# Kernel optimization log

Hardware: AMD Instinct MI355X
Metric: run time of the kernel (lower is better)

The kernel has to match this reference:

```python
import jax, jax.numpy as jnp
import numpy as np

V = 100000   # nodes
E = 3200000  # edges (avg degree 32)
K = 16       # radial filters
T = 4        # atom types


def setup_inputs() -> dict:
    key = jax.random.key(0)
    k1, k2, k3, k4 = jax.random.split(key, 4)
    feat = jax.random.randint(k1, (V, 1), 0, T).astype(jnp.float32)  # atomic-type ids as floats
    distances = jax.random.uniform(k2, (E, 1), jnp.float32) * 12.0   # pairwise distances in [0, 12)
    src = jax.random.randint(k3, (E,), 0, V, dtype=jnp.int32)
    dst = jax.random.randint(k4, (E,), 0, V, dtype=jnp.int32)
    interaction_cutoffs = jnp.full((K,), 12.0, dtype=jnp.float32)
    rbf_kernel_means = jnp.linspace(0.0, 12.0, K).astype(jnp.float32)
    rbf_kernel_scaling = jnp.ones((K,), dtype=jnp.float32)
    features_to_use = jnp.arange(T, dtype=jnp.float32)
    return {
        'feat': feat, 'distances': distances, 'src': src, 'dst': dst,
        'interaction_cutoffs': interaction_cutoffs,
        'rbf_kernel_means': rbf_kernel_means,
        'rbf_kernel_scaling': rbf_kernel_scaling,
        'features_to_use': features_to_use,
    }


def reference(feat, distances, src, dst, interaction_cutoffs,
              rbf_kernel_means, rbf_kernel_scaling, features_to_use):
    d = distances                                    # (E, 1)
    # RadialPooling: rbf * cosine cutoff, broadcast (E,1) vs (K,) -> (E,K)
    rbf = jnp.exp(-rbf_kernel_scaling * (d - rbf_kernel_means) ** 2)
    cos_v = 0.5 * (jnp.cos(jnp.pi * d / interaction_cutoffs) + 1.0)
    he = rbf * jnp.where(d <= interaction_cutoffs, cos_v, jnp.zeros_like(cos_v))  # (E, K)
    # one-hot atom-type features (V, T)
    hv = (feat == features_to_use[None, :]).astype(distances.dtype)
    # gather src features, outer product with radial features -> (E, T, K)
    msg = hv[src][:, :, None] * he[:, None, :]
    # scatter-sum to destination nodes -> (V, T*K)
    out = jax.ops.segment_sum(msg.reshape(msg.shape[0], -1), dst, num_segments=V)
    return out
```

## Files before the change

### kernel.cpp

```cpp
#include <hip/hip_runtime.h>
#include <math.h>

#define NV 100000
#define NE 3200000
#define NK 16
#define NT 4
#define NB 1563
#define NBP 1564
#define NKEY 256
#define SCH 4096
#define NCH ((NE + SCH - 1) / SCH)
#define RCAP 2432
#define CPT 4
#define NBIN 16384
#define BINSCALE (NBIN / 12.0f)
#define NVW ((NV + 15) / 16)
#define PI_F 3.14159265358979323846f

typedef float vfloat4 __attribute__((ext_vector_type(4)));
typedef int   vint4   __attribute__((ext_vector_type(4)));


__global__ __launch_bounds__(256) void zero_out_kernel(float4* __restrict__ out, int n4) {
    int i = blockIdx.x * blockDim.x + threadIdx.x;
    if (i < n4) out[i] = make_float4(0.f, 0.f, 0.f, 0.f);
}

__global__ __launch_bounds__(256) void atomic_conv_edge_kernel(
    const float* __restrict__ feat, const float* __restrict__ dist,
    const int* __restrict__ src, const int* __restrict__ dst,
    const float* __restrict__ cutoffs, const float* __restrict__ means,
    const float* __restrict__ scaling, const float* __restrict__ feats_use,
    float* __restrict__ out)
{
    int e = blockIdx.x * blockDim.x + threadIdx.x;
    if (e >= NE) return;
    float d = dist[e];
    int s = src[e];
    int v = dst[e];
    float fv = feat[s];
    int ty = 0;
#pragma unroll
    for (int t = 1; t < NT; ++t) if (fv == feats_use[t]) ty = t;
    float* o = out + (size_t)v * (NT * NK) + (size_t)ty * NK;
#pragma unroll
    for (int k = 0; k < NK; ++k) {
        float c = cutoffs[k], m = means[k], sc = scaling[k];
        float dm = d - m;
        float rbf = __expf(-sc * dm * dm);
        float cosv = 0.5f * (__cosf(PI_F * d / c) + 1.0f);
        float he = (d <= c) ? rbf * cosv : 0.0f;
        __hip_atomic_fetch_add(o + k, he, __ATOMIC_RELAXED, __HIP_MEMORY_SCOPE_AGENT);
    }
}


__global__ __launch_bounds__(256) void prep_kernel(
    const float* __restrict__ feat, const float* __restrict__ feats_use,
    const float* __restrict__ cutoffs, const float* __restrict__ means,
    const float* __restrict__ scaling,
    unsigned* __restrict__ fpk, float* __restrict__ tab)
{
    int tid = blockIdx.x * 256 + threadIdx.x;
    if (tid < NBIN * NK) {
        int bin = tid >> 4, k = tid & 15;
        float dc = ((float)bin + 0.5f) * (12.0f / NBIN);
        float c = cutoffs[k], m = means[k], sc = scaling[k];
        float dm = dc - m;
        float rbf = expf(-sc * dm * dm);
        float cosv = 0.5f * (cosf(PI_F * dc / c) + 1.0f);
        tab[tid] = (dc <= c) ? rbf * cosv : 0.0f;
    }
    if (tid < NVW) {
        float f1 = feats_use[1], f2 = feats_use[2], f3 = feats_use[3];
        unsigned w = 0;
        int base = tid * 16;
#pragma unroll
        for (int j = 0; j < 16; ++j) {
            int idx = base + j;
            float fv = (idx < NV) ? feat[idx] : -1.0f;
            unsigned ty = (fv == f1) ? 1u : (fv == f2) ? 2u : (fv == f3) ? 3u : 0u;
            w |= ty << (2 * j);
        }
        fpk[tid] = w;
    }
}


__global__ __launch_bounds__(512, 4) void scatter_kernel(
    const unsigned* __restrict__ fpk, const float* __restrict__ dist,
    const int* __restrict__ src, const int* __restrict__ dst,
    unsigned short* __restrict__ offs, unsigned* __restrict__ payload)
{
    __shared__ unsigned pld[SCH];
    __shared__ unsigned short bkt[SCH];
    __shared__ int hist[NB];
    __shared__ int wsum[8];

    int t = threadIdx.x;
    int c = blockIdx.x;
    int chunkBase = c * SCH;
    int n = NE - chunkBase;
    if (n > SCH) n = SCH;

    for (int i = t; i < NB; i += 512) hist[i] = 0;
    __syncthreads();

    int nq = n >> 2;
    const vfloat4* d4 = (const vfloat4*)(dist + chunkBase);
    const vint4*   s4 = (const vint4*)(src + chunkBase);
    const vint4*   v4 = (const vint4*)(dst + chunkBase);
    for (int i = t; i < nq; i += 512) {
        vfloat4 dd = __builtin_nontemporal_load(&d4[i]);
        vint4   ss = __builtin_nontemporal_load(&s4[i]);
        vint4   vv = __builtin_nontemporal_load(&v4[i]);
#pragma unroll
        for (int j = 0; j < 4; ++j) {
            int s = ss[j];
            unsigned w = fpk[s >> 4];
            unsigned ty = (w >> ((s & 15) << 1)) & 3u;
            int bin = (int)(dd[j] * BINSCALE);
            bin = (bin > NBIN - 1) ? NBIN - 1 : bin;
            int v = vv[j];
            pld[4 * i + j] = ((unsigned)bin << 8) | ((unsigned)(v & 63) << 2) | ty;
            bkt[4 * i + j] = (unsigned short)(v >> 6);
            atomicAdd(&hist[v >> 6], 1);
        }
    }
    for (int i = (nq << 2) + t; i < n; i += 512) {
        int e = chunkBase + i;
        int s = src[e];
        unsigned w = fpk[s >> 4];
        unsigned ty = (w >> ((s & 15) << 1)) & 3u;
        int bin = (int)(dist[e] * BINSCALE);
        bin = (bin > NBIN - 1) ? NBIN - 1 : bin;
        int v = dst[e];
        pld[i] = ((unsigned)bin << 8) | ((unsigned)(v & 63) << 2) | ty;
        bkt[i] = (unsigned short)(v >> 6);
        atomicAdd(&hist[v >> 6], 1);
    }
    __syncthreads();

    int base_i = t * CPT;
    int loc[CPT];
    int sum = 0;
#pragma unroll
    for (int i = 0; i < CPT; ++i) {
        int idx = base_i + i;
        int v = (idx < NB) ? hist[idx] : 0;
        loc[i] = sum;
        sum += v;
    }
    int lane = t & 63, wv = t >> 6;
    int inc = sum;
#pragma unroll
    for (int o = 1; o < 64; o <<= 1) {
        int u = __shfl_up(inc, o, 64);
        if (lane >= o) inc += u;
    }
    if (lane == 63) wsum[wv] = inc;
    __syncthreads();
    int add = 0;
#pragma unroll
    for (int w = 0; w < 8; ++w) add += (w < wv) ? wsum[w] : 0;
    int excl = add + inc - sum;

    unsigned short* __restrict__ oc = offs + (size_t)c * NBP;
#pragma unroll
    for (int i = 0; i < CPT; ++i) {
        int idx = base_i + i;
        int pref = excl + loc[i];
        if (idx < NB) {
            oc[idx] = (unsigned short)pref;
            hist[idx] = pref;
        } else if (idx == NB) {
            oc[NB] = (unsigned short)n;
        }
    }
    __syncthreads();

    unsigned* __restrict__ pout = payload + (size_t)chunkBase;
    for (int i = t; i < n; i += 512) {
        int b = bkt[i];
        int pos = atomicAdd(&hist[b], 1);
        pout[pos] = pld[i];
    }
}

__global__ __launch_bounds__(512, 8) void reduce_kernel(
    const unsigned* __restrict__ payload, const unsigned short* __restrict__ offs,
    const float* __restrict__ tab, float* __restrict__ out)
{
    __shared__ unsigned lds_buf[2 * RCAP];
    __shared__ int scn[NKEY];
    __shared__ int cur[NKEY];
    __shared__ int coff[NKEY + 1];
    __shared__ int wsum[4];
    __shared__ int tot;

    unsigned* raw = lds_buf;
    unsigned* srt = lds_buf + RCAP;
    float* stage = (float*)lds_buf;

    int jj = blockIdx.x;
    int xg = jj & 7, ji = jj >> 3;
    int b = ((xg < 3) ? xg * 196 : 588 + (xg - 3) * 195) + ji;
    int t = threadIdx.x;

    if (t < NKEY) scn[t] = 0;
    if (t == 0) tot = 0;
    __syncthreads();

    for (int c = t; c < NCH; c += 512) {
        const unsigned short* oc = offs + (size_t)c * NBP + b;
        int s = oc[0];
        int e = oc[1];
        int cnt = e - s;
        if (cnt > 0) {
            int pos = atomicAdd(&tot, cnt);
            if (pos + cnt > RCAP) cnt = (pos < RCAP) ? (RCAP - pos) : 0;
            const unsigned* __restrict__ pp = payload + (size_t)c * SCH + s;
            for (int q = 0; q < cnt; ++q) {
                unsigned p = pp[q];
                raw[pos + q] = p;
                atomicAdd(&scn[p & 255u], 1);
            }
        }
    }
    __syncthreads();
    int n = tot;
    if (n > RCAP) n = RCAP;

    int x = (t < NKEY) ? scn[t] : 0;
    int lane = t & 63, wv = t >> 6;
    int inc = x;
#pragma unroll
    for (int o = 1; o < 64; o <<= 1) {
        int u = __shfl_up(inc, o, 64);
        if (lane >= o) inc += u;
    }
    if (lane == 63 && t < NKEY) wsum[wv] = inc;
    __syncthreads();
    if (t < NKEY) {
        int add = 0;
#pragma unroll
        for (int w = 0; w < 4; ++w) add += (w < wv) ? wsum[w] : 0;
        int excl = add + inc - x;
        coff[t] = excl;
        cur[t] = excl;
        if (t == 255) coff[NKEY] = n;
    }
    __syncthreads();

    for (int i = t; i < n; i += 512) {
        unsigned p = raw[i];
        int pos = atomicAdd(&cur[p & 255u], 1);
        srt[pos] = p;
    }
    __syncthreads();

    float acc[NK];
#pragma unroll
    for (int k = 0; k < NK; ++k) acc[k] = 0.f;

    int key = t & 255;
    int s0 = coff[key];
    int s1 = coff[key + 1];
    int h = (s1 - s0) >> 1;
    int i0 = (t < NKEY) ? s0 : (s1 - h);
    int i1 = (t < NKEY) ? (s1 - h) : s1;

#pragma unroll 2
    for (int i = i0; i < i1; ++i) {
        unsigned p = srt[i];
        const vfloat4* row = (const vfloat4*)(tab + (size_t)((p >> 8) & 0x3FFFu) * 16);
        vfloat4 r0 = row[0], r1 = row[1], r2 = row[2], r3 = row[3];
        acc[0]  += r0.x; acc[1]  += r0.y; acc[2]  += r0.z; acc[3]  += r0.w;
        acc[4]  += r1.x; acc[5]  += r1.y; acc[6]  += r1.z; acc[7]  += r1.w;
        acc[8]  += r2.x; acc[9]  += r2.y; acc[10] += r2.z; acc[11] += r2.w;
        acc[12] += r3.x; acc[13] += r3.y; acc[14] += r3.z; acc[15] += r3.w;
    }
    __syncthreads();

    if (t >= NKEY) {
#pragma unroll
        for (int k = 0; k < NK; ++k) stage[(t - NKEY) * 17 + k] = acc[k];
    }
    __syncthreads();

    if (t < NKEY) {
#pragma unroll
        for (int k = 0; k < NK; ++k) acc[k] += stage[t * 17 + k];
        int node = b * 64 + (t >> 2);
        if (node < NV) {
            vfloat4* o = (vfloat4*)(out + (size_t)node * 64 + (size_t)(t & 3) * 16);
#pragma unroll
            for (int q = 0; q < 4; ++q) {
                vfloat4 v = {acc[4 * q], acc[4 * q + 1], acc[4 * q + 2], acc[4 * q + 3]};
                __builtin_nontemporal_store(v, &o[q]);
            }
        }
    }
}

extern "C" void kernel_launch(void* const* d_in, const int* in_sizes, int n_in,
                              void* d_out, int out_size, void* d_ws, size_t ws_size,
                              hipStream_t stream) {
    const float* feat      = (const float*)d_in[0];
    const float* dist      = (const float*)d_in[1];
    const int*   src       = (const int*)d_in[2];
    const int*   dst       = (const int*)d_in[3];
    const float* cutoffs   = (const float*)d_in[4];
    const float* means     = (const float*)d_in[5];
    const float* scaling   = (const float*)d_in[6];
    const float* feats_use = (const float*)d_in[7];
    float* out = (float*)d_out;

    size_t off = 0;
    auto alloc = [&](size_t bytes) {
        size_t cur = off;
        off = (off + bytes + 255) & ~(size_t)255;
        return cur;
    };
    size_t o_offs    = alloc((size_t)NCH * NBP * 2);
    size_t o_payload = alloc((size_t)NE * 4);
    size_t o_fpk     = alloc((size_t)NVW * 4);
    size_t o_tab     = alloc((size_t)NBIN * NK * 4);
    size_t needed = off;

    if (ws_size < needed) {
        int n4 = out_size / 4;
        zero_out_kernel<<<(n4 + 255) / 256, 256, 0, stream>>>((float4*)out, n4);
        atomic_conv_edge_kernel<<<(NE + 255) / 256, 256, 0, stream>>>(
            feat, dist, src, dst, cutoffs, means, scaling, feats_use, out);
        return;
    }

    char* ws = (char*)d_ws;
    unsigned short* offs = (unsigned short*)(ws + o_offs);
    unsigned* payload    = (unsigned*)(ws + o_payload);
    unsigned* fpk        = (unsigned*)(ws + o_fpk);
    float* tab           = (float*)(ws + o_tab);

    prep_kernel<<<(NBIN * NK) / 256, 256, 0, stream>>>(
        feat, feats_use, cutoffs, means, scaling, fpk, tab);

    scatter_kernel<<<NCH, 512, 0, stream>>>(
        fpk, dist, src, dst, offs, payload);

    reduce_kernel<<<NB, 512, 0, stream>>>(
        payload, offs, tab, out);
}
```

Baseline: 175.2 us.

## Transpose chunk offsets and reduce two buckets per block with prefix-scan placement

Adds a transpose kernel so the reduce kernel can read each bucket's per-chunk offsets contiguously instead of striding by NBP. Each reduce block now handles two adjacent buckets (512 keys, one per thread), so the cross-thread accumulator merge through LDS goes away. Write positions in LDS come from a block-wide prefix scan of per-chunk counts rather than an atomic counter. The cost is an extra kernel launch and workspace buffer, a larger LDS footprint that lowers occupancy (launch bounds 512,4), and half as many blocks.

```diff
diff --git a/kernel.cpp b/kernel.cpp
--- a/kernel.cpp
+++ b/kernel.cpp
@@ -7,10 +7,11 @@
 #define NT 4
 #define NB 1563
 #define NBP 1564
-#define NKEY 256
+#define NCHP 784
 #define SCH 4096
 #define NCH ((NE + SCH - 1) / SCH)
-#define RCAP 2432
+#define NKEY2 512
+#define RCAP2 4608
 #define CPT 4
 #define NBIN 16384
 #define BINSCALE (NBIN / 12.0f)
@@ -187,75 +188,127 @@
     }
 }
 
-__global__ __launch_bounds__(512, 8) void reduce_kernel(
-    const unsigned* __restrict__ payload, const unsigned short* __restrict__ offs,
+__global__ __launch_bounds__(256) void transpose_kernel(
+    const unsigned short* __restrict__ offs, unsigned short* __restrict__ offs_t)
+{
+    __shared__ unsigned short tile[64][65];
+    int t = threadIdx.x;
+    int tb = t & 63, tq = t >> 6;
+    int b0 = blockIdx.x * 64, c0 = blockIdx.y * 64;
+#pragma unroll
+    for (int r = 0; r < 16; ++r) {
+        int c = c0 + tq * 16 + r;
+        int b = b0 + tb;
+        tile[tq * 16 + r][tb] =
+            (c < NCH && b < NB + 1) ? offs[(size_t)c * NBP + b] : (unsigned short)0;
+    }
+    __syncthreads();
+#pragma unroll
+    for (int r = 0; r < 16; ++r) {
+        int b = b0 + tq * 16 + r;
+        int c = c0 + tb;
+        if (b < NB + 1 && c < NCH)
+            offs_t[(size_t)b * NCHP + c] = tile[tb][tq * 16 + r];
+    }
+}
+
+__global__ __launch_bounds__(512, 4) void reduce_kernel(
+    const unsigned* __restrict__ payload, const unsigned short* __restrict__ offs_t,
     const float* __restrict__ tab, float* __restrict__ out)
 {
-    __shared__ unsigned lds_buf[2 * RCAP];
-    __shared__ int scn[NKEY];
-    __shared__ int cur[NKEY];
-    __shared__ int coff[NKEY + 1];
-    __shared__ int wsum[4];
-    __shared__ int tot;
-
-    unsigned* raw = lds_buf;
-    unsigned* srt = lds_buf + RCAP;
-    float* stage = (float*)lds_buf;
-
+    __shared__ unsigned short rows[3][NCHP];
+    __shared__ unsigned raw[RCAP2];
+    __shared__ unsigned srt[RCAP2];
+    __shared__ int scn[NKEY2];
+    __shared__ int cur[NKEY2];
+    __shared__ int coff[NKEY2 + 1];
+    __shared__ int wsum[8];
+    __shared__ int ntot;
+
+    int t = threadIdx.x;
     int jj = blockIdx.x;
     int xg = jj & 7, ji = jj >> 3;
-    int b = ((xg < 3) ? xg * 196 : 588 + (xg - 3) * 195) + ji;
-    int t = threadIdx.x;
-
-    if (t < NKEY) scn[t] = 0;
-    if (t == 0) tot = 0;
-    __syncthreads();
-
-    for (int c = t; c < NCH; c += 512) {
-        const unsigned short* oc = offs + (size_t)c * NBP + b;
-        int s = oc[0];
-        int e = oc[1];
-        int cnt = e - s;
-        if (cnt > 0) {
-            int pos = atomicAdd(&tot, cnt);
-            if (pos + cnt > RCAP) cnt = (pos < RCAP) ? (RCAP - pos) : 0;
-            const unsigned* __restrict__ pp = payload + (size_t)c * SCH + s;
-            for (int q = 0; q < cnt; ++q) {
-                unsigned p = pp[q];
-                raw[pos + q] = p;
-                atomicAdd(&scn[p & 255u], 1);
-            }
-        }
-    }
-    __syncthreads();
-    int n = tot;
-    if (n > RCAP) n = RCAP;
-
-    int x = (t < NKEY) ? scn[t] : 0;
+    int pi = ((xg < 6) ? xg * 98 : 588 + (xg - 6) * 97) + ji;
+    int b0 = pi * 2;
+    bool has2 = (b0 + 1 < NB);
+
+    for (int i = t; i < 3 * NCHP; i += 512) {
+        int rr = i / NCHP, cc = i - rr * NCHP;
+        int br = b0 + rr;
+        rows[rr][cc] = (cc < NCH && br <= NB) ? offs_t[(size_t)br * NCHP + cc]
+                                              : (unsigned short)0;
+    }
+    scn[t] = 0;
+    __syncthreads();
+
+    int myS[2], myM[2], myE[2];
+    int cnt = 0;
+#pragma unroll
+    for (int j = 0; j < 2; ++j) {
+        int c = t + j * 512;
+        myS[j] = 0; myM[j] = 0; myE[j] = 0;
+        if (c < NCH) {
+            int s = rows[0][c];
+            int m = rows[1][c];
+            int e = has2 ? rows[2][c] : m;
+            myS[j] = s; myM[j] = m; myE[j] = e;
+            cnt += e - s;
+        }
+    }
     int lane = t & 63, wv = t >> 6;
-    int inc = x;
+    int inc = cnt;
 #pragma unroll
     for (int o = 1; o < 64; o <<= 1) {
         int u = __shfl_up(inc, o, 64);
         if (lane >= o) inc += u;
     }
-    if (lane == 63 && t < NKEY) wsum[wv] = inc;
-    __syncthreads();
-    if (t < NKEY) {
-        int add = 0;
-#pragma unroll
-        for (int w = 0; w < 4; ++w) add += (w < wv) ? wsum[w] : 0;
-        int excl = add + inc - x;
-        coff[t] = excl;
-        cur[t] = excl;
-        if (t == 255) coff[NKEY] = n;
-    }
+    if (lane == 63) wsum[wv] = inc;
+    __syncthreads();
+    int add = 0;
+#pragma unroll
+    for (int w = 0; w < 8; ++w) add += (w < wv) ? wsum[w] : 0;
+    int pos = add + inc - cnt;
+    if (t == 511) ntot = add + inc;
+
+#pragma unroll
+    for (int j = 0; j < 2; ++j) {
+        int c = t + j * 512;
+        if (c >= NCH) break;
+        const unsigned* __restrict__ pp = payload + (size_t)c * SCH;
+        for (int q = myS[j]; q < myE[j]; ++q) {
+            if (pos >= RCAP2) break;
+            unsigned p = pp[q];
+            if (q >= myM[j]) p |= (1u << 22);
+            raw[pos++] = p;
+            atomicAdd(&scn[(int)(((p >> 14) & 256u) | (p & 255u))], 1);
+        }
+    }
+    __syncthreads();
+    int n = ntot;
+    if (n > RCAP2) n = RCAP2;
+
+    int x = scn[t];
+    inc = x;
+#pragma unroll
+    for (int o = 1; o < 64; o <<= 1) {
+        int u = __shfl_up(inc, o, 64);
+        if (lane >= o) inc += u;
+    }
+    if (lane == 63) wsum[wv] = inc;
+    __syncthreads();
+    add = 0;
+#pragma unroll
+    for (int w = 0; w < 8; ++w) add += (w < wv) ? wsum[w] : 0;
+    int excl = add + inc - x;
+    coff[t] = excl;
+    cur[t] = excl;
+    if (t == 511) coff[NKEY2] = n;
     __syncthreads();
 
     for (int i = t; i < n; i += 512) {
         unsigned p = raw[i];
-        int pos = atomicAdd(&cur[p & 255u], 1);
-        srt[pos] = p;
+        int ps = atomicAdd(&cur[(int)(((p >> 14) & 256u) | (p & 255u))], 1);
+        srt[ps] = p;
     }
     __syncthreads();
 
@@ -263,15 +316,10 @@
 #pragma unroll
     for (int k = 0; k < NK; ++k) acc[k] = 0.f;
 
-    int key = t & 255;
-    int s0 = coff[key];
-    int s1 = coff[key + 1];
-    int h = (s1 - s0) >> 1;
-    int i0 = (t < NKEY) ? s0 : (s1 - h);
-    int i1 = (t < NKEY) ? (s1 - h) : s1;
-
+    int e0 = coff[t];
+    int e1 = coff[t + 1];
 #pragma unroll 2
-    for (int i = i0; i < i1; ++i) {
+    for (int i = e0; i < e1; ++i) {
         unsigned p = srt[i];
         const vfloat4* row = (const vfloat4*)(tab + (size_t)((p >> 8) & 0x3FFFu) * 16);
         vfloat4 r0 = row[0], r1 = row[1], r2 = row[2], r3 = row[3];
@@ -280,25 +328,14 @@
         acc[8]  += r2.x; acc[9]  += r2.y; acc[10] += r2.z; acc[11] += r2.w;
         acc[12] += r3.x; acc[13] += r3.y; acc[14] += r3.z; acc[15] += r3.w;
     }
-    __syncthreads();
-
-    if (t >= NKEY) {
-#pragma unroll
-        for (int k = 0; k < NK; ++k) stage[(t - NKEY) * 17 + k] = acc[k];
-    }
-    __syncthreads();
-
-    if (t < NKEY) {
-#pragma unroll
-        for (int k = 0; k < NK; ++k) acc[k] += stage[t * 17 + k];
-        int node = b * 64 + (t >> 2);
-        if (node < NV) {
-            vfloat4* o = (vfloat4*)(out + (size_t)node * 64 + (size_t)(t & 3) * 16);
-#pragma unroll
-            for (int q = 0; q < 4; ++q) {
-                vfloat4 v = {acc[4 * q], acc[4 * q + 1], acc[4 * q + 2], acc[4 * q + 3]};
-                __builtin_nontemporal_store(v, &o[q]);
-            }
+
+    int node = b0 * 64 + (t >> 2);
+    if (node < NV) {
+        vfloat4* o = (vfloat4*)(out + (size_t)node * 64 + (size_t)(t & 3) * 16);
+#pragma unroll
+        for (int q = 0; q < 4; ++q) {
+            vfloat4 v = {acc[4 * q], acc[4 * q + 1], acc[4 * q + 2], acc[4 * q + 3]};
+            __builtin_nontemporal_store(v, &o[q]);
         }
     }
 }
@@ -323,6 +360,7 @@
         return cur;
     };
     size_t o_offs    = alloc((size_t)NCH * NBP * 2);
+    size_t o_offs_t  = alloc((size_t)(NB + 1) * NCHP * 2);
     size_t o_payload = alloc((size_t)NE * 4);
     size_t o_fpk     = alloc((size_t)NVW * 4);
     size_t o_tab     = alloc((size_t)NBIN * NK * 4);
@@ -337,10 +375,11 @@
     }
 
     char* ws = (char*)d_ws;
-    unsigned short* offs = (unsigned short*)(ws + o_offs);
-    unsigned* payload    = (unsigned*)(ws + o_payload);
-    unsigned* fpk        = (unsigned*)(ws + o_fpk);
-    float* tab           = (float*)(ws + o_tab);
+    unsigned short* offs   = (unsigned short*)(ws + o_offs);
+    unsigned short* offs_t = (unsigned short*)(ws + o_offs_t);
+    unsigned* payload      = (unsigned*)(ws + o_payload);
+    unsigned* fpk          = (unsigned*)(ws + o_fpk);
+    float* tab             = (float*)(ws + o_tab);
 
     prep_kernel<<<(NBIN * NK) / 256, 256, 0, stream>>>(
         feat, feats_use, cutoffs, means, scaling, fpk, tab);
@@ -348,6 +387,9 @@
     scatter_kernel<<<NCH, 512, 0, stream>>>(
         fpk, dist, src, dst, offs, payload);
 
-    reduce_kernel<<<NB, 512, 0, stream>>>(
-        payload, offs, tab, out);
-}
+    dim3 tg((NB + 1 + 63) / 64, (NCH + 63) / 64);
+    transpose_kernel<<<tg, 256, 0, stream>>>(offs, offs_t);
+
+    reduce_kernel<<<(NB + 1) / 2, 512, 0, stream>>>(
+        payload, offs_t, tab, out);
+}
```

New measurement: 185.8 us. 1.06x slower.
